# Performance work log

Measured on AMD Instinct MI355X. Metric: run time of the kernel, lower is better.

## Reference

```python
import jax, jax.numpy as jnp
import numpy as np

ATOM_FDIM = 35
BOND_FDIM = 5
MAX_NB = 10
HIDDEN = 128
DEPTH = 6
N_ATOMS = 100000
N_BONDS = 220000
N_MESS = 20000
N_MOLS = 2000


def setup_inputs() -> dict:
    key = jax.random.key(0)
    ks = jax.random.split(key, 10)
    fatoms = jax.random.uniform(ks[0], (N_ATOMS, ATOM_FDIM), dtype=jnp.float32)
    fbonds = jax.random.uniform(ks[1], (N_BONDS, ATOM_FDIM + BOND_FDIM), dtype=jnp.float32)
    tree_message = jax.random.normal(ks[2], (N_MESS, HIDDEN), dtype=jnp.float32)
    tree_message = tree_message.at[0].set(0.0)  # index 0 is the zero-padding message
    agraph = jax.random.randint(ks[3], (N_ATOMS, MAX_NB), 0, N_MESS + N_BONDS, dtype=jnp.int32)
    bgraph = jax.random.randint(ks[4], (N_BONDS, MAX_NB), 0, N_MESS + N_BONDS, dtype=jnp.int32)
    mol_ids = jnp.sort(jax.random.randint(ks[5], (N_ATOMS,), 0, N_MOLS, dtype=jnp.int32))
    # learned parameters (torch Linear stores W as [out, in]; we keep [in, out])
    def lin(k, fan_in, fan_out):
        bound = 1.0 / np.sqrt(fan_in)
        return jax.random.uniform(k, (fan_in, fan_out), minval=-bound, maxval=bound, dtype=jnp.float32)
    W_i = lin(ks[6], ATOM_FDIM + BOND_FDIM, HIDDEN)
    W_h = lin(ks[7], HIDDEN, HIDDEN)
    W_o = lin(ks[8], ATOM_FDIM + HIDDEN, HIDDEN)
    b_o = jax.random.uniform(ks[9], (HIDDEN,), minval=-1.0 / np.sqrt(ATOM_FDIM + HIDDEN), maxval=1.0 / np.sqrt(ATOM_FDIM + HIDDEN), dtype=jnp.float32)
    return {
        'fatoms': fatoms, 'fbonds': fbonds, 'tree_message': tree_message,
        'agraph': agraph, 'bgraph': bgraph, 'mol_ids': mol_ids, 'n_mols': N_MOLS,
        'W_i': W_i, 'W_h': W_h, 'W_o': W_o, 'b_o': b_o,
    }


def reference(fatoms, fbonds, tree_message, agraph, bgraph, mol_ids, n_mols, W_i, W_h, W_o, b_o):
    binput = fbonds @ W_i                    # [B, H]
    graph_message = jax.nn.relu(binput)
    for _ in range(DEPTH - 1):
        message = jnp.concatenate([tree_message, graph_message], axis=0)  # [M+B, H]
        nei = message[bgraph].sum(axis=1)    # gather [B, MAX_NB, H] -> sum -> [B, H]
        graph_message = jax.nn.relu(binput + nei @ W_h)
    message = jnp.concatenate([tree_message, graph_message], axis=0)
    nei_a = message[agraph].sum(axis=1)      # [A, H]
    ainput = jnp.concatenate([fatoms, nei_a], axis=1)  # [A, ATOM_FDIM+H]
    atom_hiddens = jax.nn.relu(ainput @ W_o + b_o)     # [A, H]
    # mean-pool per molecule (scope)
    sums = jax.ops.segment_sum(atom_hiddens, mol_ids, num_segments=n_mols)
    counts = jax.ops.segment_sum(jnp.ones((atom_hiddens.shape[0],), dtype=atom_hiddens.dtype), mol_ids, num_segments=n_mols)
    mol_vecs = sums / jnp.maximum(counts, 1.0)[:, None]
    return mol_vecs
```

## Files before the change

kernel.cpp:

```cpp
#include <hip/hip_runtime.h>

#define N_ATOMS   100000
#define N_BONDS   220000
#define N_MESS    20000
#define N_MSG     (N_MESS + N_BONDS)
#define ATOM_FDIM 35
#define BOND_FDIM 5
#define BOND_IN   (ATOM_FDIM + BOND_FDIM)
#define H         128
#define MAX_NB    10
#define DEPTH     6
#define KO        (ATOM_FDIM + H)
#define KC        192

typedef __attribute__((ext_vector_type(8))) short short8;
typedef __attribute__((ext_vector_type(4))) float f32x4;

static __device__ __forceinline__ float asf(unsigned int u) {
    union { unsigned int i; float f; } v; v.i = u; return v.f;
}
static __device__ __forceinline__ float bflo(unsigned int v) { return asf(v << 16); }
static __device__ __forceinline__ float bfhi(unsigned int v) { return asf(v & 0xffff0000u); }

static __device__ __forceinline__ unsigned short f2bf(float f) {
    union { float f; unsigned int i; } v; v.f = f;
    unsigned int x = v.i;
    return (unsigned short)((x + 0x7FFFu + ((x >> 16) & 1u)) >> 16);
}

#define PT0 (N_MESS * H)
#define PT1 (PT0 + N_BONDS * BOND_IN)
#define PT2 (PT1 + H * KC)
#define PT3 (PT2 + H * KC)

__global__ __launch_bounds__(256) void prep(
    const float* __restrict__ tree, const float* __restrict__ fbonds,
    const float* __restrict__ Wi, const float* __restrict__ Wh,
    const float* __restrict__ Wo,
    ushort* __restrict__ msgA, ushort* __restrict__ msgB,
    ushort* __restrict__ fbc, ushort* __restrict__ WT,
    ushort* __restrict__ WoT, float* __restrict__ out, int n_out)
{
    int i = blockIdx.x * 256 + threadIdx.x;
    if (i < PT0) {
        unsigned short v = f2bf(tree[i]);
        msgA[i] = v; msgB[i] = v;
    } else if (i < PT1) {
        int j = i - PT0;
        fbc[j] = f2bf(fbonds[j]);
    } else if (i < PT2) {
        int j = i - PT1;
        int n = j / KC, k = j - n * KC;
        float v = (k < BOND_IN) ? Wi[k * H + n]
                : (k < BOND_IN + H) ? Wh[(k - BOND_IN) * H + n] : 0.f;
        WT[j] = f2bf(v);
    } else if (i < PT3) {
        int j = i - PT2;
        int n = j / KC, k = j - n * KC;
        float v = (k < H) ? Wo[(ATOM_FDIM + k) * H + n]
                : (k < KO) ? Wo[(k - H) * H + n] : 0.f;
        WoT[j] = f2bf(v);
    } else {
        int j = i - PT3;
        if (j < n_out) out[j] = 0.f;
    }
}

__global__ __launch_bounds__(256, 4) void binput0(
    const ushort* __restrict__ fbc, const ushort* __restrict__ WT,
    ushort* __restrict__ gout)
{
    __shared__ ushort Xlds[32 * 25 * 8];

    int tid = threadIdx.x;
    int bond0 = blockIdx.x * 32;
    int lane = tid & 63, wv = tid >> 6;

    if (tid < 160) {
        int b = tid / 5, k8 = tid - b * 5;
        *(short8*)&Xlds[(b * 25 + k8) * 8] =
            *(const short8*)&fbc[(size_t)bond0 * BOND_IN + tid * 8];
    }
    if (tid < 96) {
        int b = tid / 3, k8 = 5 + (tid - b * 3);
        *(float4*)&Xlds[(b * 25 + k8) * 8] = float4{0.f, 0.f, 0.f, 0.f};
    }
    __syncthreads();

    int n0 = wv * 32;
    int m_lane = lane & 15, quad = lane >> 4;
    f32x4 c00 = {0,0,0,0}, c01 = {0,0,0,0}, c10 = {0,0,0,0}, c11 = {0,0,0,0};

    #pragma unroll
    for (int s = 0; s < 2; s++) {
        short8 a0 = *(const short8*)&Xlds[((m_lane)      * 25 + s * 4 + quad) * 8];
        short8 a1 = *(const short8*)&Xlds[((16 + m_lane) * 25 + s * 4 + quad) * 8];
        short8 b0 = *(const short8*)&WT[(size_t)(n0 + m_lane)      * KC + s * 32 + quad * 8];
        short8 b1 = *(const short8*)&WT[(size_t)(n0 + 16 + m_lane) * KC + s * 32 + quad * 8];
        c00 = __builtin_amdgcn_mfma_f32_16x16x32_bf16(a0, b0, c00, 0, 0, 0);
        c01 = __builtin_amdgcn_mfma_f32_16x16x32_bf16(a0, b1, c01, 0, 0, 0);
        c10 = __builtin_amdgcn_mfma_f32_16x16x32_bf16(a1, b0, c10, 0, 0, 0);
        c11 = __builtin_amdgcn_mfma_f32_16x16x32_bf16(a1, b1, c11, 0, 0, 0);
    }

    #pragma unroll
    for (int r = 0; r < 4; r++) {
        int row0 = bond0 + quad * 4 + r;
        int row1 = row0 + 16;
        gout[(size_t)row0 * H + n0 + m_lane]      = f2bf(fmaxf(c00[r], 0.f));
        gout[(size_t)row0 * H + n0 + 16 + m_lane] = f2bf(fmaxf(c01[r], 0.f));
        gout[(size_t)row1 * H + n0 + m_lane]      = f2bf(fmaxf(c10[r], 0.f));
        gout[(size_t)row1 * H + n0 + 16 + m_lane] = f2bf(fmaxf(c11[r], 0.f));
    }
}

__global__ __launch_bounds__(256, 4) void mp_round(
    const ushort* __restrict__ msg_in, const ushort* __restrict__ fbc,
    const int* __restrict__ bgraph, const ushort* __restrict__ WT,
    ushort* __restrict__ graph_out)
{
    __shared__ ushort Xlds[32 * 25 * 8];

    int tid = threadIdx.x;
    int bond0 = blockIdx.x * 32;
    int lane = tid & 63, wv = tid >> 6;
    int q = lane >> 4, c16 = lane & 15;

    if (tid < 160) {
        int b = tid / 5, k8 = tid - b * 5;
        *(short8*)&Xlds[(b * 25 + k8) * 8] =
            *(const short8*)&fbc[(size_t)bond0 * BOND_IN + tid * 8];
    }
    if (tid < 96) {
        int b = tid / 3, k8 = 21 + (tid - b * 3);
        *(float4*)&Xlds[(b * 25 + k8) * 8] = float4{0.f, 0.f, 0.f, 0.f};
    }
    #pragma unroll
    for (int g = 0; g < 2; g++) {
        int b = wv + 4 * (g * 4 + q);
        const int* bg = bgraph + (size_t)(bond0 + b) * MAX_NB;
        int idx[MAX_NB];
        #pragma unroll
        for (int n = 0; n < MAX_NB; n++) idx[n] = bg[n];
        uint4 v[MAX_NB];
        #pragma unroll
        for (int n = 0; n < MAX_NB; n++)
            v[n] = *(const uint4*)(msg_in + (size_t)idx[n] * H + c16 * 8);
        float s0=0.f,s1=0.f,s2=0.f,s3=0.f,s4=0.f,s5=0.f,s6=0.f,s7=0.f;
        #pragma unroll
        for (int n = 0; n < MAX_NB; n++) {
            s0 += bflo(v[n].x); s1 += bfhi(v[n].x);
            s2 += bflo(v[n].y); s3 += bfhi(v[n].y);
            s4 += bflo(v[n].z); s5 += bfhi(v[n].z);
            s6 += bflo(v[n].w); s7 += bfhi(v[n].w);
        }
        uint4 pk;
        pk.x = ((unsigned int)f2bf(s1) << 16) | (unsigned int)f2bf(s0);
        pk.y = ((unsigned int)f2bf(s3) << 16) | (unsigned int)f2bf(s2);
        pk.z = ((unsigned int)f2bf(s5) << 16) | (unsigned int)f2bf(s4);
        pk.w = ((unsigned int)f2bf(s7) << 16) | (unsigned int)f2bf(s6);
        *(uint4*)&Xlds[(b * 25 + 5 + c16) * 8] = pk;
    }
    __syncthreads();

    int n0 = wv * 32;
    int m_lane = lane & 15, quad = lane >> 4;
    f32x4 c00 = {0,0,0,0}, c01 = {0,0,0,0}, c10 = {0,0,0,0}, c11 = {0,0,0,0};

    #pragma unroll
    for (int s = 0; s < KC / 32; s++) {
        short8 a0 = *(const short8*)&Xlds[((m_lane)      * 25 + s * 4 + quad) * 8];
        short8 a1 = *(const short8*)&Xlds[((16 + m_lane) * 25 + s * 4 + quad) * 8];
        short8 b0 = *(const short8*)&WT[(size_t)(n0 + m_lane)      * KC + s * 32 + quad * 8];
        short8 b1 = *(const short8*)&WT[(size_t)(n0 + 16 + m_lane) * KC + s * 32 + quad * 8];
        c00 = __builtin_amdgcn_mfma_f32_16x16x32_bf16(a0, b0, c00, 0, 0, 0);
        c01 = __builtin_amdgcn_mfma_f32_16x16x32_bf16(a0, b1, c01, 0, 0, 0);
        c10 = __builtin_amdgcn_mfma_f32_16x16x32_bf16(a1, b0, c10, 0, 0, 0);
        c11 = __builtin_amdgcn_mfma_f32_16x16x32_bf16(a1, b1, c11, 0, 0, 0);
    }

    #pragma unroll
    for (int r = 0; r < 4; r++) {
        int row0 = bond0 + quad * 4 + r;
        int row1 = row0 + 16;
        graph_out[(size_t)row0 * H + n0 + m_lane]      = f2bf(fmaxf(c00[r], 0.f));
        graph_out[(size_t)row0 * H + n0 + 16 + m_lane] = f2bf(fmaxf(c01[r], 0.f));
        graph_out[(size_t)row1 * H + n0 + m_lane]      = f2bf(fmaxf(c10[r], 0.f));
        graph_out[(size_t)row1 * H + n0 + 16 + m_lane] = f2bf(fmaxf(c11[r], 0.f));
    }
}

__global__ __launch_bounds__(256, 4) void atom_mfma(
    const float* __restrict__ fatoms, const ushort* __restrict__ msg,
    const int* __restrict__ agraph, const ushort* __restrict__ WoT,
    const float* __restrict__ bo, const int* __restrict__ mol_ids,
    float* __restrict__ out)
{
    __shared__ ushort Xlds[32 * 25 * 8];
    __shared__ float htile[32 * H];
    __shared__ int mlds[32];

    int tid = threadIdx.x;
    int a0 = blockIdx.x * 32;
    int lane = tid & 63, wv = tid >> 6;
    int q = lane >> 4, c16 = lane & 15;

    for (int i = tid; i < 32 * ATOM_FDIM; i += 256) {
        int b = i / ATOM_FDIM, t = i - b * ATOM_FDIM;
        int k = H + t;
        Xlds[(b * 25 + (k >> 3)) * 8 + (k & 7)] = f2bf(fatoms[(size_t)a0 * ATOM_FDIM + i]);
    }
    if (tid < 160) {
        int b = tid / 5, k = 163 + (tid - b * 5);
        Xlds[(b * 25 + (k >> 3)) * 8 + (k & 7)] = 0;
    }
    if (tid < 96) {
        int b = tid / 3, k8 = 21 + (tid - b * 3);
        *(float4*)&Xlds[(b * 25 + k8) * 8] = float4{0.f, 0.f, 0.f, 0.f};
    }
    if (tid < 32) mlds[tid] = mol_ids[a0 + tid];
    #pragma unroll
    for (int g = 0; g < 2; g++) {
        int b = wv + 4 * (g * 4 + q);
        const int* ag = agraph + (size_t)(a0 + b) * MAX_NB;
        int idx[MAX_NB];
        #pragma unroll
        for (int n = 0; n < MAX_NB; n++) idx[n] = ag[n];
        uint4 v[MAX_NB];
        #pragma unroll
        for (int n = 0; n < MAX_NB; n++)
            v[n] = *(const uint4*)(msg + (size_t)idx[n] * H + c16 * 8);
        float s0=0.f,s1=0.f,s2=0.f,s3=0.f,s4=0.f,s5=0.f,s6=0.f,s7=0.f;
        #pragma unroll
        for (int n = 0; n < MAX_NB; n++) {
            s0 += bflo(v[n].x); s1 += bfhi(v[n].x);
            s2 += bflo(v[n].y); s3 += bfhi(v[n].y);
            s4 += bflo(v[n].z); s5 += bfhi(v[n].z);
            s6 += bflo(v[n].w); s7 += bfhi(v[n].w);
        }
        uint4 pk;
        pk.x = ((unsigned int)f2bf(s1) << 16) | (unsigned int)f2bf(s0);
        pk.y = ((unsigned int)f2bf(s3) << 16) | (unsigned int)f2bf(s2);
        pk.z = ((unsigned int)f2bf(s5) << 16) | (unsigned int)f2bf(s4);
        pk.w = ((unsigned int)f2bf(s7) << 16) | (unsigned int)f2bf(s6);
        *(uint4*)&Xlds[(b * 25 + c16) * 8] = pk;
    }
    __syncthreads();

    int n0 = wv * 32;
    int m_lane = lane & 15, quad = lane >> 4;
    float bias0 = bo[n0 + m_lane], bias1 = bo[n0 + 16 + m_lane];
    f32x4 c00 = {bias0, bias0, bias0, bias0};
    f32x4 c01 = {bias1, bias1, bias1, bias1};
    f32x4 c10 = {bias0, bias0, bias0, bias0};
    f32x4 c11 = {bias1, bias1, bias1, bias1};

    #pragma unroll
    for (int s = 0; s < KC / 32; s++) {
        short8 a0f = *(const short8*)&Xlds[((m_lane)      * 25 + s * 4 + quad) * 8];
        short8 a1f = *(const short8*)&Xlds[((16 + m_lane) * 25 + s * 4 + quad) * 8];
        short8 b0f = *(const short8*)&WoT[(size_t)(n0 + m_lane)      * KC + s * 32 + quad * 8];
        short8 b1f = *(const short8*)&WoT[(size_t)(n0 + 16 + m_lane) * KC + s * 32 + quad * 8];
        c00 = __builtin_amdgcn_mfma_f32_16x16x32_bf16(a0f, b0f, c00, 0, 0, 0);
        c01 = __builtin_amdgcn_mfma_f32_16x16x32_bf16(a0f, b1f, c01, 0, 0, 0);
        c10 = __builtin_amdgcn_mfma_f32_16x16x32_bf16(a1f, b0f, c10, 0, 0, 0);
        c11 = __builtin_amdgcn_mfma_f32_16x16x32_bf16(a1f, b1f, c11, 0, 0, 0);
    }

    #pragma unroll
    for (int r = 0; r < 4; r++) {
        int r0 = quad * 4 + r, r1 = r0 + 16;
        htile[r0 * H + n0 + m_lane]      = fmaxf(c00[r], 0.f);
        htile[r0 * H + n0 + 16 + m_lane] = fmaxf(c01[r], 0.f);
        htile[r1 * H + n0 + m_lane]      = fmaxf(c10[r], 0.f);
        htile[r1 * H + n0 + 16 + m_lane] = fmaxf(c11[r], 0.f);
    }
    __syncthreads();

    if (tid < H) {
        int j = tid;
        float acc = 0.f;
        int cur = mlds[0];
        for (int r = 0; r < 32; r++) {
            int m = mlds[r];
            if (m != cur) {
                atomicAdd(&out[(size_t)cur * H + j], acc);
                acc = 0.f; cur = m;
            }
            acc += htile[r * H + j];
        }
        atomicAdd(&out[(size_t)cur * H + j], acc);
    }
}

__global__ __launch_bounds__(128) void pool_div(
    const int* __restrict__ mol_ids, float* __restrict__ out, int n_atoms)
{
    int m = blockIdx.x;
    int j = threadIdx.x;

    int lo = 0, hi = n_atoms;
    while (lo < hi) { int mid = (lo + hi) >> 1; if (mol_ids[mid] < m) lo = mid + 1; else hi = mid; }
    int start = lo;
    hi = n_atoms;
    while (lo < hi) { int mid = (lo + hi) >> 1; if (mol_ids[mid] < m + 1) lo = mid + 1; else hi = mid; }
    int end = lo;

    out[(size_t)m * H + j] /= fmaxf((float)(end - start), 1.f);
}

extern "C" void kernel_launch(void* const* d_in, const int* in_sizes, int n_in,
                              void* d_out, int out_size, void* d_ws, size_t ws_size,
                              hipStream_t stream)
{
    const float* fatoms  = (const float*)d_in[0];
    const float* fbonds  = (const float*)d_in[1];
    const float* tree    = (const float*)d_in[2];
    const int*   agraph  = (const int*)d_in[3];
    const int*   bgraph  = (const int*)d_in[4];
    const int*   mol_ids = (const int*)d_in[5];
    const float* W_i = (const float*)d_in[7];
    const float* W_h = (const float*)d_in[8];
    const float* W_o = (const float*)d_in[9];
    const float* b_o = (const float*)d_in[10];
    float* out = (float*)d_out;

    ushort* msgA = (ushort*)d_ws;
    ushort* msgB = msgA + (size_t)N_MSG * H;
    ushort* WT   = msgB + (size_t)N_MSG * H;
    ushort* WoT  = WT + (size_t)H * KC;
    ushort* fbc  = WoT + (size_t)H * KC;

    int prep_total = PT3 + out_size;
    prep<<<(prep_total + 255) / 256, 256, 0, stream>>>(
        tree, fbonds, W_i, W_h, W_o, msgA, msgB, fbc, WT, WoT, out, out_size);

    binput0<<<N_BONDS / 32, 256, 0, stream>>>(fbc, WT, msgA + (size_t)N_MESS * H);

    const ushort* min_ = msgA; ushort* mout = msgB;
    for (int r = 0; r < DEPTH - 1; r++) {
        mp_round<<<N_BONDS / 32, 256, 0, stream>>>(min_, fbc, bgraph, WT,
                                                   mout + (size_t)N_MESS * H);
        const ushort* t = min_; min_ = mout; mout = (ushort*)t;
    }

    atom_mfma<<<N_ATOMS / 32, 256, 0, stream>>>(fatoms, min_, agraph, WoT, b_o,
                                                mol_ids, out);

    int n_mols = out_size / H;
    pool_div<<<n_mols, 128, 0, stream>>>(mol_ids, out, N_ATOMS);
}
```

Measured before the change: 665.8 us.

## Store messages as per-row 8-bit quantized values with scale/offset

Replaces the bf16 message buffers with uint8 values plus a per-row (scale, offset) pair. Tree messages are quantized with min/max in a new kernel. Graph messages are quantized in a shared epilogue that takes a per-row max across waves through LDS. Gathers now read 8 bytes plus a float2 per neighbor instead of 16 bytes, halving the random-access traffic that dominates the message-passing rounds. In exchange it adds two block syncs per tile and much larger quantization error, which risks failing the accuracy tolerance.

```diff
diff --git a/kernel.cpp b/kernel.cpp
--- a/kernel.cpp
+++ b/kernel.cpp
@@ -16,61 +16,171 @@
 typedef __attribute__((ext_vector_type(8))) short short8;
 typedef __attribute__((ext_vector_type(4))) float f32x4;
 
-static __device__ __forceinline__ float asf(unsigned int u) {
-    union { unsigned int i; float f; } v; v.i = u; return v.f;
-}
-static __device__ __forceinline__ float bflo(unsigned int v) { return asf(v << 16); }
-static __device__ __forceinline__ float bfhi(unsigned int v) { return asf(v & 0xffff0000u); }
-
 static __device__ __forceinline__ unsigned short f2bf(float f) {
     union { float f; unsigned int i; } v; v.f = f;
     unsigned int x = v.i;
     return (unsigned short)((x + 0x7FFFu + ((x >> 16) & 1u)) >> 16);
 }
 
-#define PT0 (N_MESS * H)
-#define PT1 (PT0 + N_BONDS * BOND_IN)
-#define PT2 (PT1 + H * KC)
-#define PT3 (PT2 + H * KC)
+static __device__ __forceinline__ float ub2f(unsigned int v, int b) {
+    return (float)((v >> (b * 8)) & 0xffu);
+}
+
+static __device__ __forceinline__ unsigned char q8(float x) {
+    int q = __float2int_rn(x);
+    q = q < 0 ? 0 : (q > 255 ? 255 : q);
+    return (unsigned char)q;
+}
+
+#define PTa (N_BONDS * BOND_IN)
+#define PTb (PTa + H * KC)
+#define PTc (PTb + H * KC)
 
 __global__ __launch_bounds__(256) void prep(
-    const float* __restrict__ tree, const float* __restrict__ fbonds,
+    const float* __restrict__ fbonds,
     const float* __restrict__ Wi, const float* __restrict__ Wh,
     const float* __restrict__ Wo,
-    ushort* __restrict__ msgA, ushort* __restrict__ msgB,
     ushort* __restrict__ fbc, ushort* __restrict__ WT,
     ushort* __restrict__ WoT, float* __restrict__ out, int n_out)
 {
     int i = blockIdx.x * 256 + threadIdx.x;
-    if (i < PT0) {
-        unsigned short v = f2bf(tree[i]);
-        msgA[i] = v; msgB[i] = v;
-    } else if (i < PT1) {
-        int j = i - PT0;
-        fbc[j] = f2bf(fbonds[j]);
-    } else if (i < PT2) {
-        int j = i - PT1;
+    if (i < PTa) {
+        fbc[i] = f2bf(fbonds[i]);
+    } else if (i < PTb) {
+        int j = i - PTa;
         int n = j / KC, k = j - n * KC;
         float v = (k < BOND_IN) ? Wi[k * H + n]
                 : (k < BOND_IN + H) ? Wh[(k - BOND_IN) * H + n] : 0.f;
         WT[j] = f2bf(v);
-    } else if (i < PT3) {
-        int j = i - PT2;
+    } else if (i < PTc) {
+        int j = i - PTb;
         int n = j / KC, k = j - n * KC;
         float v = (k < H) ? Wo[(ATOM_FDIM + k) * H + n]
                 : (k < KO) ? Wo[(k - H) * H + n] : 0.f;
         WoT[j] = f2bf(v);
     } else {
-        int j = i - PT3;
+        int j = i - PTc;
         if (j < n_out) out[j] = 0.f;
+    }
+}
+
+__global__ __launch_bounds__(256) void qtree(
+    const float* __restrict__ tree,
+    unsigned char* __restrict__ qA, unsigned char* __restrict__ qB,
+    float2* __restrict__ sA, float2* __restrict__ sB)
+{
+    int row = blockIdx.x * 4 + (threadIdx.x >> 6);
+    int lane = threadIdx.x & 63;
+    float2 v = *(const float2*)&tree[(size_t)row * H + lane * 2];
+    float mx = fmaxf(v.x, v.y), mn = fminf(v.x, v.y);
+    #pragma unroll
+    for (int d = 1; d <= 32; d <<= 1) {
+        mx = fmaxf(mx, __shfl_xor(mx, d));
+        mn = fminf(mn, __shfl_xor(mn, d));
+    }
+    float rng = mx - mn;
+    float inv = (rng > 0.f) ? 255.f / rng : 0.f;
+    int q0 = q8((v.x - mn) * inv);
+    int q1 = q8((v.y - mn) * inv);
+    unsigned short pk = (unsigned short)(q0 | (q1 << 8));
+    ((unsigned short*)qA)[(size_t)row * 64 + lane] = pk;
+    ((unsigned short*)qB)[(size_t)row * 64 + lane] = pk;
+    if (lane == 0) {
+        float2 s = make_float2(rng * (1.f / 255.f), mn);
+        sA[row] = s; sB[row] = s;
+    }
+}
+
+static __device__ __forceinline__ uint4 gather8(
+    const unsigned char* __restrict__ msgq, const float2* __restrict__ scl,
+    const int* __restrict__ gidx, int c16)
+{
+    int idx[MAX_NB];
+    #pragma unroll
+    for (int n = 0; n < MAX_NB; n++) idx[n] = gidx[n];
+    float2 so[MAX_NB];
+    uint2 d[MAX_NB];
+    #pragma unroll
+    for (int n = 0; n < MAX_NB; n++) {
+        so[n] = scl[idx[n]];
+        d[n] = *(const uint2*)(msgq + (size_t)idx[n] * H + c16 * 8);
+    }
+    float s0=0.f,s1=0.f,s2=0.f,s3=0.f,s4=0.f,s5=0.f,s6=0.f,s7=0.f;
+    float off = 0.f;
+    #pragma unroll
+    for (int n = 0; n < MAX_NB; n++) {
+        float sc = so[n].x; off += so[n].y;
+        s0 += sc * ub2f(d[n].x, 0); s1 += sc * ub2f(d[n].x, 1);
+        s2 += sc * ub2f(d[n].x, 2); s3 += sc * ub2f(d[n].x, 3);
+        s4 += sc * ub2f(d[n].y, 0); s5 += sc * ub2f(d[n].y, 1);
+        s6 += sc * ub2f(d[n].y, 2); s7 += sc * ub2f(d[n].y, 3);
+    }
+    s0 += off; s1 += off; s2 += off; s3 += off;
+    s4 += off; s5 += off; s6 += off; s7 += off;
+    uint4 pk;
+    pk.x = ((unsigned)f2bf(s1) << 16) | (unsigned)f2bf(s0);
+    pk.y = ((unsigned)f2bf(s3) << 16) | (unsigned)f2bf(s2);
+    pk.z = ((unsigned)f2bf(s5) << 16) | (unsigned)f2bf(s4);
+    pk.w = ((unsigned)f2bf(s7) << 16) | (unsigned)f2bf(s6);
+    return pk;
+}
+
+static __device__ __forceinline__ void quant_epilogue(
+    f32x4 c00, f32x4 c01, f32x4 c10, f32x4 c11,
+    int tid, int row_base,
+    float* rmx, float* qp,
+    unsigned char* __restrict__ gq, float2* __restrict__ scout)
+{
+    int lane = tid & 63, wv = tid >> 6;
+    int m_lane = lane & 15, quad = lane >> 4;
+    int n0 = wv * 32;
+
+    float v00[4], v01[4], v10[4], v11[4];
+    #pragma unroll
+    for (int r = 0; r < 4; r++) {
+        v00[r] = fmaxf(c00[r], 0.f); v01[r] = fmaxf(c01[r], 0.f);
+        v10[r] = fmaxf(c10[r], 0.f); v11[r] = fmaxf(c11[r], 0.f);
+    }
+    #pragma unroll
+    for (int r = 0; r < 4; r++) {
+        float mx0 = fmaxf(v00[r], v01[r]);
+        float mx1 = fmaxf(v10[r], v11[r]);
+        #pragma unroll
+        for (int d = 1; d <= 8; d <<= 1) {
+            mx0 = fmaxf(mx0, __shfl_xor(mx0, d));
+            mx1 = fmaxf(mx1, __shfl_xor(mx1, d));
+        }
+        if (m_lane == 0) {
+            rmx[(quad * 4 + r) * 4 + wv]      = mx0;
+            rmx[(quad * 4 + r + 16) * 4 + wv] = mx1;
+        }
+    }
+    __syncthreads();
+    if (tid < 32) {
+        float mx = fmaxf(fmaxf(rmx[tid * 4], rmx[tid * 4 + 1]),
+                         fmaxf(rmx[tid * 4 + 2], rmx[tid * 4 + 3]));
+        qp[tid] = (mx > 0.f) ? 255.f / mx : 0.f;
+        scout[row_base + tid] = make_float2(mx * (1.f / 255.f), 0.f);
+    }
+    __syncthreads();
+    #pragma unroll
+    for (int r = 0; r < 4; r++) {
+        int r0 = quad * 4 + r, r1 = r0 + 16;
+        float i0 = qp[r0], i1 = qp[r1];
+        gq[(size_t)(row_base + r0) * H + n0 + m_lane]      = q8(v00[r] * i0);
+        gq[(size_t)(row_base + r0) * H + n0 + 16 + m_lane] = q8(v01[r] * i0);
+        gq[(size_t)(row_base + r1) * H + n0 + m_lane]      = q8(v10[r] * i1);
+        gq[(size_t)(row_base + r1) * H + n0 + 16 + m_lane] = q8(v11[r] * i1);
     }
 }
 
 __global__ __launch_bounds__(256, 4) void binput0(
     const ushort* __restrict__ fbc, const ushort* __restrict__ WT,
-    ushort* __restrict__ gout)
+    unsigned char* __restrict__ gq_out, float2* __restrict__ sc_out)
 {
     __shared__ ushort Xlds[32 * 25 * 8];
+    __shared__ float rmx[32 * 4];
+    __shared__ float qp[32];
 
     int tid = threadIdx.x;
     int bond0 = blockIdx.x * 32;
@@ -103,23 +213,18 @@
         c11 = __builtin_amdgcn_mfma_f32_16x16x32_bf16(a1, b1, c11, 0, 0, 0);
     }
 
-    #pragma unroll
-    for (int r = 0; r < 4; r++) {
-        int row0 = bond0 + quad * 4 + r;
-        int row1 = row0 + 16;
-        gout[(size_t)row0 * H + n0 + m_lane]      = f2bf(fmaxf(c00[r], 0.f));
-        gout[(size_t)row0 * H + n0 + 16 + m_lane] = f2bf(fmaxf(c01[r], 0.f));
-        gout[(size_t)row1 * H + n0 + m_lane]      = f2bf(fmaxf(c10[r], 0.f));
-        gout[(size_t)row1 * H + n0 + 16 + m_lane] = f2bf(fmaxf(c11[r], 0.f));
-    }
+    quant_epilogue(c00, c01, c10, c11, tid, bond0, rmx, qp, gq_out, sc_out);
 }
 
 __global__ __launch_bounds__(256, 4) void mp_round(
-    const ushort* __restrict__ msg_in, const ushort* __restrict__ fbc,
-    const int* __restrict__ bgraph, const ushort* __restrict__ WT,
-    ushort* __restrict__ graph_out)
+    const unsigned char* __restrict__ msg_in, const float2* __restrict__ sc_in,
+    const ushort* __restrict__ fbc, const int* __restrict__ bgraph,
+    const ushort* __restrict__ WT,
+    unsigned char* __restrict__ gq_out, float2* __restrict__ sc_out)
 {
     __shared__ ushort Xlds[32 * 25 * 8];
+    __shared__ float rmx[32 * 4];
+    __shared__ float qp[32];
 
     int tid = threadIdx.x;
     int bond0 = blockIdx.x * 32;
@@ -138,27 +243,7 @@
     #pragma unroll
     for (int g = 0; g < 2; g++) {
         int b = wv + 4 * (g * 4 + q);
-        const int* bg = bgraph + (size_t)(bond0 + b) * MAX_NB;
-        int idx[MAX_NB];
-        #pragma unroll
-        for (int n = 0; n < MAX_NB; n++) idx[n] = bg[n];
-        uint4 v[MAX_NB];
-        #pragma unroll
-        for (int n = 0; n < MAX_NB; n++)
-            v[n] = *(const uint4*)(msg_in + (size_t)idx[n] * H + c16 * 8);
-        float s0=0.f,s1=0.f,s2=0.f,s3=0.f,s4=0.f,s5=0.f,s6=0.f,s7=0.f;
-        #pragma unroll
-        for (int n = 0; n < MAX_NB; n++) {
-            s0 += bflo(v[n].x); s1 += bfhi(v[n].x);
-            s2 += bflo(v[n].y); s3 += bfhi(v[n].y);
-            s4 += bflo(v[n].z); s5 += bfhi(v[n].z);
-            s6 += bflo(v[n].w); s7 += bfhi(v[n].w);
-        }
-        uint4 pk;
-        pk.x = ((unsigned int)f2bf(s1) << 16) | (unsigned int)f2bf(s0);
-        pk.y = ((unsigned int)f2bf(s3) << 16) | (unsigned int)f2bf(s2);
-        pk.z = ((unsigned int)f2bf(s5) << 16) | (unsigned int)f2bf(s4);
-        pk.w = ((unsigned int)f2bf(s7) << 16) | (unsigned int)f2bf(s6);
+        uint4 pk = gather8(msg_in, sc_in, bgraph + (size_t)(bond0 + b) * MAX_NB, c16);
         *(uint4*)&Xlds[(b * 25 + 5 + c16) * 8] = pk;
     }
     __syncthreads();
@@ -179,19 +264,12 @@
         c11 = __builtin_amdgcn_mfma_f32_16x16x32_bf16(a1, b1, c11, 0, 0, 0);
     }
 
-    #pragma unroll
-    for (int r = 0; r < 4; r++) {
-        int row0 = bond0 + quad * 4 + r;
-        int row1 = row0 + 16;
-        graph_out[(size_t)row0 * H + n0 + m_lane]      = f2bf(fmaxf(c00[r], 0.f));
-        graph_out[(size_t)row0 * H + n0 + 16 + m_lane] = f2bf(fmaxf(c01[r], 0.f));
-        graph_out[(size_t)row1 * H + n0 + m_lane]      = f2bf(fmaxf(c10[r], 0.f));
-        graph_out[(size_t)row1 * H + n0 + 16 + m_lane] = f2bf(fmaxf(c11[r], 0.f));
-    }
+    quant_epilogue(c00, c01, c10, c11, tid, bond0, rmx, qp, gq_out, sc_out);
 }
 
 __global__ __launch_bounds__(256, 4) void atom_mfma(
-    const float* __restrict__ fatoms, const ushort* __restrict__ msg,
+    const float* __restrict__ fatoms, const unsigned char* __restrict__ msg,
+    const float2* __restrict__ scl,
     const int* __restrict__ agraph, const ushort* __restrict__ WoT,
     const float* __restrict__ bo, const int* __restrict__ mol_ids,
     float* __restrict__ out)
@@ -222,27 +300,7 @@
     #pragma unroll
     for (int g = 0; g < 2; g++) {
         int b = wv + 4 * (g * 4 + q);
-        const int* ag = agraph + (size_t)(a0 + b) * MAX_NB;
-        int idx[MAX_NB];
-        #pragma unroll
-        for (int n = 0; n < MAX_NB; n++) idx[n] = ag[n];
-        uint4 v[MAX_NB];
-        #pragma unroll
-        for (int n = 0; n < MAX_NB; n++)
-            v[n] = *(const uint4*)(msg + (size_t)idx[n] * H + c16 * 8);
-        float s0=0.f,s1=0.f,s2=0.f,s3=0.f,s4=0.f,s5=0.f,s6=0.f,s7=0.f;
-        #pragma unroll
-        for (int n = 0; n < MAX_NB; n++) {
-            s0 += bflo(v[n].x); s1 += bfhi(v[n].x);
-            s2 += bflo(v[n].y); s3 += bfhi(v[n].y);
-            s4 += bflo(v[n].z); s5 += bfhi(v[n].z);
-            s6 += bflo(v[n].w); s7 += bfhi(v[n].w);
-        }
-        uint4 pk;
-        pk.x = ((unsigned int)f2bf(s1) << 16) | (unsigned int)f2bf(s0);
-        pk.y = ((unsigned int)f2bf(s3) << 16) | (unsigned int)f2bf(s2);
-        pk.z = ((unsigned int)f2bf(s5) << 16) | (unsigned int)f2bf(s4);
-        pk.w = ((unsigned int)f2bf(s7) << 16) | (unsigned int)f2bf(s6);
+        uint4 pk = gather8(msg, scl, agraph + (size_t)(a0 + b) * MAX_NB, c16);
         *(uint4*)&Xlds[(b * 25 + c16) * 8] = pk;
     }
     __syncthreads();
@@ -325,26 +383,33 @@
     const float* b_o = (const float*)d_in[10];
     float* out = (float*)d_out;
 
-    ushort* msgA = (ushort*)d_ws;
-    ushort* msgB = msgA + (size_t)N_MSG * H;
-    ushort* WT   = msgB + (size_t)N_MSG * H;
-    ushort* WoT  = WT + (size_t)H * KC;
-    ushort* fbc  = WoT + (size_t)H * KC;
-
-    int prep_total = PT3 + out_size;
+    unsigned char* mqA = (unsigned char*)d_ws;
+    unsigned char* mqB = mqA + (size_t)N_MSG * H;
+    float2* scA = (float2*)(mqB + (size_t)N_MSG * H);
+    float2* scB = scA + N_MSG;
+    ushort* WT  = (ushort*)(scB + N_MSG);
+    ushort* WoT = WT + (size_t)H * KC;
+    ushort* fbc = WoT + (size_t)H * KC;
+
+    int prep_total = PTc + out_size;
     prep<<<(prep_total + 255) / 256, 256, 0, stream>>>(
-        tree, fbonds, W_i, W_h, W_o, msgA, msgB, fbc, WT, WoT, out, out_size);
-
-    binput0<<<N_BONDS / 32, 256, 0, stream>>>(fbc, WT, msgA + (size_t)N_MESS * H);
-
-    const ushort* min_ = msgA; ushort* mout = msgB;
+        fbonds, W_i, W_h, W_o, fbc, WT, WoT, out, out_size);
+
+    qtree<<<N_MESS / 4, 256, 0, stream>>>(tree, mqA, mqB, scA, scB);
+
+    binput0<<<N_BONDS / 32, 256, 0, stream>>>(fbc, WT,
+        mqA + (size_t)N_MESS * H, scA + N_MESS);
+
+    const unsigned char* tin = mqA; const float2* sin = scA;
+    unsigned char* tout = mqB; float2* sout = scB;
     for (int r = 0; r < DEPTH - 1; r++) {
-        mp_round<<<N_BONDS / 32, 256, 0, stream>>>(min_, fbc, bgraph, WT,
-                                                   mout + (size_t)N_MESS * H);
-        const ushort* t = min_; min_ = mout; mout = (ushort*)t;
-    }
-
-    atom_mfma<<<N_ATOMS / 32, 256, 0, stream>>>(fatoms, min_, agraph, WoT, b_o,
+        mp_round<<<N_BONDS / 32, 256, 0, stream>>>(tin, sin, fbc, bgraph, WT,
+            tout + (size_t)N_MESS * H, sout + N_MESS);
+        const unsigned char* t1 = tin; tin = tout; tout = (unsigned char*)t1;
+        const float2* t2 = sin; sin = sout; sout = (float2*)t2;
+    }
+
+    atom_mfma<<<N_ATOMS / 32, 256, 0, stream>>>(fatoms, tin, sin, agraph, WoT, b_o,
                                                 mol_ids, out);
 
     int n_mols = out_size / H;
```

Result: faster. 626.6 us (-5.9%).
